# Kernel optimization log

Measured on AMD Instinct MI355X. Metric: run time of the kernel, lower is better.

Reference implementation:

```python
import jax, jax.numpy as jnp
import numpy as np

WIN = (9, 9)
EPS = float(np.power(np.e, -15))  # e^-15 threshold from original code


def _box_sum(x, win):
    kernel = jnp.ones((1, 1, win[0], win[1]), dtype=x.dtype)
    p = win[0] // 2
    return jax.lax.conv_general_dilated(
        x, kernel, window_strides=(1, 1), padding=[(p, p), (p, p)],
        dimension_numbers=("NCHW", "OIHW", "NCHW"))


def setup_inputs() -> dict:
    key = jax.random.key(0)
    k1, k2 = jax.random.split(key)
    B, C, H, W = 32, 1, 512, 512
    I = jax.random.normal(k1, (B, C, H, W), dtype=jnp.float32)
    J = jax.random.normal(k2, (B, C, H, W), dtype=jnp.float32)
    return {"I": I, "J": J}


def reference(I, J):
    win = WIN
    win_size = win[0] * win[1]
    I_sum = _box_sum(I, win)
    J_sum = _box_sum(J, win)
    I2_sum = _box_sum(I * I, win)
    J2_sum = _box_sum(J * J, win)
    IJ_sum = _box_sum(I * J, win)

    u_I = I_sum / win_size
    u_J = J_sum / win_size
    cross = IJ_sum - u_J * I_sum - u_I * J_sum + u_I * u_J * win_size
    I_var = I2_sum - 2 * u_I * I_sum + u_I * u_I * win_size
    J_var = J2_sum - 2 * u_J * J_sum + u_J * u_J * win_size

    non_zero = I_var * J_var > EPS
    cross = jnp.where(non_zero, cross, 1.0)
    I_var = jnp.where(non_zero, I_var, 1.0)
    J_var = jnp.where(non_zero, J_var, 1.0)

    cc = cross * cross / (I_var * J_var + EPS)
    return -1.0 * jnp.mean(cc, axis=(1, 2, 3)) + 1.0
```

## Files before the change

### kernel.cpp

```cpp
#include <hip/hip_runtime.h>


#define IMG_H 512
#define IMG_W 512
#define NBATCH 32
#define RPW 16
#define STRIPS_PER_IMG (IMG_H / RPW)
#define RING 10

typedef __attribute__((address_space(3))) void       lds_t;
typedef __attribute__((address_space(1))) const void glob_t;

__global__ __launch_bounds__(64, 1) void lcc_main(const float* __restrict__ I,
                                                  const float* __restrict__ J,
                                                  float* __restrict__ out) {
    __shared__ __align__(16) float ring[RING][1024];

    const int lane  = threadIdx.x;
    const int strip = blockIdx.x;
    const int b  = strip >> 5;
    const int y0 = (strip & 31) * RPW;
    const int x0 = lane * 8;

    const float* __restrict__ Ib = I + (size_t)b * IMG_H * IMG_W;
    const float* __restrict__ Jb = J + (size_t)b * IMG_H * IMG_W;

    auto issue_row = [&](int y) {
        int slot = (y - y0 + 4) % RING;
        const float* gI = Ib + y * IMG_W;
        const float* gJ = Jb + y * IMG_W;
        float* lI = &ring[slot][0];
        float* lJ = &ring[slot][512];
        __builtin_amdgcn_global_load_lds((glob_t*)(gI +       lane * 4), (lds_t*)lI,         16, 0, 0);
        __builtin_amdgcn_global_load_lds((glob_t*)(gI + 256 + lane * 4), (lds_t*)(lI + 256), 16, 0, 0);
        __builtin_amdgcn_global_load_lds((glob_t*)(gJ +       lane * 4), (lds_t*)lJ,         16, 0, 0);
        __builtin_amdgcn_global_load_lds((glob_t*)(gJ + 256 + lane * 4), (lds_t*)(lJ + 256), 16, 0, 0);
    };

    float sI[8]  = {0.f,0.f,0.f,0.f,0.f,0.f,0.f,0.f};
    float sJ[8]  = {0.f,0.f,0.f,0.f,0.f,0.f,0.f,0.f};
    float sII[8] = {0.f,0.f,0.f,0.f,0.f,0.f,0.f,0.f};
    float sJJ[8] = {0.f,0.f,0.f,0.f,0.f,0.f,0.f,0.f};
    float sIJ[8] = {0.f,0.f,0.f,0.f,0.f,0.f,0.f,0.f};

    auto add_ld = [&](int y) {
        int slot = (y - y0 + 4) % RING;
        const float4* pI = reinterpret_cast<const float4*>(&ring[slot][x0]);
        const float4* pJ = reinterpret_cast<const float4*>(&ring[slot][512 + x0]);
        float4 i0 = pI[0], i1 = pI[1], j0 = pJ[0], j1 = pJ[1];
        float iv[8] = {i0.x,i0.y,i0.z,i0.w,i1.x,i1.y,i1.z,i1.w};
        float jv[8] = {j0.x,j0.y,j0.z,j0.w,j1.x,j1.y,j1.z,j1.w};
        #pragma unroll
        for (int c = 0; c < 8; ++c) {
            sI[c]  += iv[c];
            sJ[c]  += jv[c];
            sII[c]  = fmaf(iv[c], iv[c], sII[c]);
            sJJ[c]  = fmaf(jv[c], jv[c], sJJ[c]);
            sIJ[c]  = fmaf(iv[c], jv[c], sIJ[c]);
        }
    };
    auto sub_ld = [&](int y) {
        int slot = (y - y0 + 4) % RING;
        const float4* pI = reinterpret_cast<const float4*>(&ring[slot][x0]);
        const float4* pJ = reinterpret_cast<const float4*>(&ring[slot][512 + x0]);
        float4 i0 = pI[0], i1 = pI[1], j0 = pJ[0], j1 = pJ[1];
        float iv[8] = {i0.x,i0.y,i0.z,i0.w,i1.x,i1.y,i1.z,i1.w};
        float jv[8] = {j0.x,j0.y,j0.z,j0.w,j1.x,j1.y,j1.z,j1.w};
        #pragma unroll
        for (int c = 0; c < 8; ++c) {
            sI[c]  -= iv[c];
            sJ[c]  -= jv[c];
            sII[c]  = fmaf(-iv[c], iv[c], sII[c]);
            sJJ[c]  = fmaf(-jv[c], jv[c], sJJ[c]);
            sIJ[c]  = fmaf(-iv[c], jv[c], sIJ[c]);
        }
    };

    auto hsum = [&](const float (&s)[8], float (&h)[8]) {
        float w[16];
        #pragma unroll
        for (int c = 0; c < 8; ++c) w[4+c] = s[c];
        #pragma unroll
        for (int c = 0; c < 4; ++c) {
            float a = __shfl_up(s[4+c], 1);
            w[c] = lane ? a : 0.f;
            a = __shfl_down(s[c], 1);
            w[12+c] = (lane < 63) ? a : 0.f;
        }
        float acc = 0.f;
        #pragma unroll
        for (int i = 0; i < 9; ++i) acc += w[i];
        h[0] = acc;
        #pragma unroll
        for (int k = 1; k < 8; ++k) { acc += w[k+8] - w[k-1]; h[k] = acc; }
    };

    const int wy_lo = (y0 - 4 < 0) ? 0 : y0 - 4;
    const int wy_hi = y0 + 4;
    #pragma unroll 1
    for (int y = wy_lo; y <= wy_hi; ++y) issue_row(y);
    __builtin_amdgcn_s_waitcnt(0x3F70);
    #pragma unroll 1
    for (int y = wy_lo; y <= wy_hi; ++y) add_ld(y);

    const float inv81 = 1.0f / 81.0f;
    const float EPSV  = 3.0590232050182579e-07f;
    float local = 0.0f;

    #pragma unroll 1
    for (int r = 0; r < RPW; ++r) {
        const int t = y0 + r;

        const bool pf = (r + 1 < RPW) && (t + 5 < IMG_H);
        if (pf) {
            __builtin_amdgcn_s_waitcnt(0xC07F);
            issue_row(t + 5);
        }

        float hI[8], hJ[8], hII[8], hJJ[8], hIJ[8];
        hsum(sI,  hI);
        hsum(sJ,  hJ);
        hsum(sII, hII);
        hsum(sJJ, hJJ);
        hsum(sIJ, hIJ);

        #pragma unroll
        for (int k = 0; k < 8; ++k) {
            float cross = fmaf(hI[k] * hJ[k], -inv81, hIJ[k]);
            float Iv    = fmaf(hI[k] * hI[k], -inv81, hII[k]);
            float Jv    = fmaf(hJ[k] * hJ[k], -inv81, hJJ[k]);
            float p  = Iv * Jv;
            bool  nz = p > EPSV;
            float c2 = nz ? cross : 1.0f;
            float p2 = nz ? p : 1.0f;
            local += (c2 * c2) * __builtin_amdgcn_rcpf(p2 + EPSV);
        }

        if (r + 1 < RPW) {
            if (pf) __builtin_amdgcn_s_waitcnt(0x3F70);
            if (t + 5 < IMG_H) add_ld(t + 5);
            if (t - 4 >= 0)    sub_ld(t - 4);
        }
    }

    #pragma unroll
    for (int off = 32; off > 0; off >>= 1) local += __shfl_down(local, off);
    if (lane == 0)
        atomicAdd(out + b, fmaf(local, -1.0f / (float)(IMG_H * IMG_W),
                                1.0f / (float)STRIPS_PER_IMG));
}

extern "C" void kernel_launch(void* const* d_in, const int* in_sizes, int n_in,
                              void* d_out, int out_size, void* d_ws, size_t ws_size,
                              hipStream_t stream) {
    const float* I = (const float*)d_in[0];
    const float* J = (const float*)d_in[1];
    float* out = (float*)d_out;

    const int total_strips = NBATCH * STRIPS_PER_IMG;
    lcc_main<<<total_strips, 64, 0, stream>>>(I, J, out);
}
```

Measured before the change: 108.0 us.

## Split each strip across two waves with LDS halo columns and barriers

Each block now runs 128 threads. Each of the two waves handles 256 columns at 4 columns per lane instead of one wave handling 512 columns at 8 per lane. The lane at each half's boundary keeps extra running sums for the 4 halo columns read from the shared LDS ring. Only wave 0 issues the global-to-LDS row loads, and __syncthreads replaces the per-wave waitcnt so wave 1 sees the data. The goal is more waves per CU and half the per-wave arithmetic and register use, at the cost of two block barriers per row and some divergent edge-lane work.

```diff
diff --git a/kernel.cpp b/kernel.cpp
--- a/kernel.cpp
+++ b/kernel.cpp
@@ -11,16 +11,21 @@
 typedef __attribute__((address_space(3))) void       lds_t;
 typedef __attribute__((address_space(1))) const void glob_t;
 
-__global__ __launch_bounds__(64, 1) void lcc_main(const float* __restrict__ I,
-                                                  const float* __restrict__ J,
-                                                  float* __restrict__ out) {
+__global__ __launch_bounds__(128, 2) void lcc_main(const float* __restrict__ I,
+                                                   const float* __restrict__ J,
+                                                   float* __restrict__ out) {
     __shared__ __align__(16) float ring[RING][1024];
 
-    const int lane  = threadIdx.x;
+    const int tid   = threadIdx.x;
+    const int lane  = tid & 63;
+    const int wid   = tid >> 6;
     const int strip = blockIdx.x;
     const int b  = strip >> 5;
     const int y0 = (strip & 31) * RPW;
-    const int x0 = lane * 8;
+    const int cb = (wid << 8) + lane * 4;
+    const bool w0 = (wid == 0);
+    const int elane = w0 ? 63 : 0;
+    const int ecol  = w0 ? 256 : 252;
 
     const float* __restrict__ Ib = I + (size_t)b * IMG_H * IMG_W;
     const float* __restrict__ Jb = J + (size_t)b * IMG_H * IMG_W;
@@ -37,69 +42,97 @@
         __builtin_amdgcn_global_load_lds((glob_t*)(gJ + 256 + lane * 4), (lds_t*)(lJ + 256), 16, 0, 0);
     };
 
-    float sI[8]  = {0.f,0.f,0.f,0.f,0.f,0.f,0.f,0.f};
-    float sJ[8]  = {0.f,0.f,0.f,0.f,0.f,0.f,0.f,0.f};
-    float sII[8] = {0.f,0.f,0.f,0.f,0.f,0.f,0.f,0.f};
-    float sJJ[8] = {0.f,0.f,0.f,0.f,0.f,0.f,0.f,0.f};
-    float sIJ[8] = {0.f,0.f,0.f,0.f,0.f,0.f,0.f,0.f};
+    float sI[4]={0,0,0,0}, sJ[4]={0,0,0,0}, sII[4]={0,0,0,0},
+          sJJ[4]={0,0,0,0}, sIJ[4]={0,0,0,0};
+    float eI[4]={0,0,0,0}, eJ[4]={0,0,0,0}, eII[4]={0,0,0,0},
+          eJJ[4]={0,0,0,0}, eIJ[4]={0,0,0,0};
 
     auto add_ld = [&](int y) {
         int slot = (y - y0 + 4) % RING;
-        const float4* pI = reinterpret_cast<const float4*>(&ring[slot][x0]);
-        const float4* pJ = reinterpret_cast<const float4*>(&ring[slot][512 + x0]);
-        float4 i0 = pI[0], i1 = pI[1], j0 = pJ[0], j1 = pJ[1];
-        float iv[8] = {i0.x,i0.y,i0.z,i0.w,i1.x,i1.y,i1.z,i1.w};
-        float jv[8] = {j0.x,j0.y,j0.z,j0.w,j1.x,j1.y,j1.z,j1.w};
+        float4 i0 = *reinterpret_cast<const float4*>(&ring[slot][cb]);
+        float4 j0 = *reinterpret_cast<const float4*>(&ring[slot][512 + cb]);
+        float iv[4] = {i0.x,i0.y,i0.z,i0.w};
+        float jv[4] = {j0.x,j0.y,j0.z,j0.w};
         #pragma unroll
-        for (int c = 0; c < 8; ++c) {
+        for (int c = 0; c < 4; ++c) {
             sI[c]  += iv[c];
             sJ[c]  += jv[c];
             sII[c]  = fmaf(iv[c], iv[c], sII[c]);
             sJJ[c]  = fmaf(jv[c], jv[c], sJJ[c]);
             sIJ[c]  = fmaf(iv[c], jv[c], sIJ[c]);
         }
+        if (lane == elane) {
+            float4 hi = *reinterpret_cast<const float4*>(&ring[slot][ecol]);
+            float4 hj = *reinterpret_cast<const float4*>(&ring[slot][512 + ecol]);
+            float xi[4] = {hi.x,hi.y,hi.z,hi.w};
+            float xj[4] = {hj.x,hj.y,hj.z,hj.w};
+            #pragma unroll
+            for (int c = 0; c < 4; ++c) {
+                eI[c]  += xi[c];
+                eJ[c]  += xj[c];
+                eII[c]  = fmaf(xi[c], xi[c], eII[c]);
+                eJJ[c]  = fmaf(xj[c], xj[c], eJJ[c]);
+                eIJ[c]  = fmaf(xi[c], xj[c], eIJ[c]);
+            }
+        }
     };
     auto sub_ld = [&](int y) {
         int slot = (y - y0 + 4) % RING;
-        const float4* pI = reinterpret_cast<const float4*>(&ring[slot][x0]);
-        const float4* pJ = reinterpret_cast<const float4*>(&ring[slot][512 + x0]);
-        float4 i0 = pI[0], i1 = pI[1], j0 = pJ[0], j1 = pJ[1];
-        float iv[8] = {i0.x,i0.y,i0.z,i0.w,i1.x,i1.y,i1.z,i1.w};
-        float jv[8] = {j0.x,j0.y,j0.z,j0.w,j1.x,j1.y,j1.z,j1.w};
+        float4 i0 = *reinterpret_cast<const float4*>(&ring[slot][cb]);
+        float4 j0 = *reinterpret_cast<const float4*>(&ring[slot][512 + cb]);
+        float iv[4] = {i0.x,i0.y,i0.z,i0.w};
+        float jv[4] = {j0.x,j0.y,j0.z,j0.w};
         #pragma unroll
-        for (int c = 0; c < 8; ++c) {
+        for (int c = 0; c < 4; ++c) {
             sI[c]  -= iv[c];
             sJ[c]  -= jv[c];
             sII[c]  = fmaf(-iv[c], iv[c], sII[c]);
             sJJ[c]  = fmaf(-jv[c], jv[c], sJJ[c]);
             sIJ[c]  = fmaf(-iv[c], jv[c], sIJ[c]);
         }
+        if (lane == elane) {
+            float4 hi = *reinterpret_cast<const float4*>(&ring[slot][ecol]);
+            float4 hj = *reinterpret_cast<const float4*>(&ring[slot][512 + ecol]);
+            float xi[4] = {hi.x,hi.y,hi.z,hi.w};
+            float xj[4] = {hj.x,hj.y,hj.z,hj.w};
+            #pragma unroll
+            for (int c = 0; c < 4; ++c) {
+                eI[c]  -= xi[c];
+                eJ[c]  -= xj[c];
+                eII[c]  = fmaf(-xi[c], xi[c], eII[c]);
+                eJJ[c]  = fmaf(-xj[c], xj[c], eJJ[c]);
+                eIJ[c]  = fmaf(-xi[c], xj[c], eIJ[c]);
+            }
+        }
     };
 
-    auto hsum = [&](const float (&s)[8], float (&h)[8]) {
-        float w[16];
-        #pragma unroll
-        for (int c = 0; c < 8; ++c) w[4+c] = s[c];
+    auto hsum = [&](const float (&s)[4], const float (&e)[4], float (&h)[4]) {
+        float w[12];
+        w[4]=s[0]; w[5]=s[1]; w[6]=s[2]; w[7]=s[3];
         #pragma unroll
         for (int c = 0; c < 4; ++c) {
-            float a = __shfl_up(s[4+c], 1);
-            w[c] = lane ? a : 0.f;
-            a = __shfl_down(s[c], 1);
-            w[12+c] = (lane < 63) ? a : 0.f;
+            float u = __shfl_up(s[c], 1);
+            float d = __shfl_down(s[c], 1);
+            w[c]   = w0 ? (lane ? u : 0.f)
+                        : (lane ? u : e[c]);
+            w[8+c] = w0 ? ((lane < 63) ? d : e[c])
+                        : ((lane < 63) ? d : 0.f);
         }
         float acc = 0.f;
         #pragma unroll
         for (int i = 0; i < 9; ++i) acc += w[i];
         h[0] = acc;
         #pragma unroll
-        for (int k = 1; k < 8; ++k) { acc += w[k+8] - w[k-1]; h[k] = acc; }
+        for (int k = 1; k < 4; ++k) { acc += w[k+8] - w[k-1]; h[k] = acc; }
     };
 
     const int wy_lo = (y0 - 4 < 0) ? 0 : y0 - 4;
     const int wy_hi = y0 + 4;
-    #pragma unroll 1
-    for (int y = wy_lo; y <= wy_hi; ++y) issue_row(y);
-    __builtin_amdgcn_s_waitcnt(0x3F70);
+    if (w0) {
+        #pragma unroll 1
+        for (int y = wy_lo; y <= wy_hi; ++y) issue_row(y);
+    }
+    __syncthreads();
     #pragma unroll 1
     for (int y = wy_lo; y <= wy_hi; ++y) add_ld(y);
 
@@ -110,22 +143,22 @@
     #pragma unroll 1
     for (int r = 0; r < RPW; ++r) {
         const int t = y0 + r;
+        const bool pf = (r + 1 < RPW) && (t + 5 < IMG_H);
 
-        const bool pf = (r + 1 < RPW) && (t + 5 < IMG_H);
-        if (pf) {
+        if (pf && w0) {
             __builtin_amdgcn_s_waitcnt(0xC07F);
             issue_row(t + 5);
         }
 
-        float hI[8], hJ[8], hII[8], hJJ[8], hIJ[8];
-        hsum(sI,  hI);
-        hsum(sJ,  hJ);
-        hsum(sII, hII);
-        hsum(sJJ, hJJ);
-        hsum(sIJ, hIJ);
+        float hI[4], hJ[4], hII[4], hJJ[4], hIJ[4];
+        hsum(sI,  eI,  hI);
+        hsum(sJ,  eJ,  hJ);
+        hsum(sII, eII, hII);
+        hsum(sJJ, eJJ, hJJ);
+        hsum(sIJ, eIJ, hIJ);
 
         #pragma unroll
-        for (int k = 0; k < 8; ++k) {
+        for (int k = 0; k < 4; ++k) {
             float cross = fmaf(hI[k] * hJ[k], -inv81, hIJ[k]);
             float Iv    = fmaf(hI[k] * hI[k], -inv81, hII[k]);
             float Jv    = fmaf(hJ[k] * hJ[k], -inv81, hJJ[k]);
@@ -137,9 +170,12 @@
         }
 
         if (r + 1 < RPW) {
-            if (pf) __builtin_amdgcn_s_waitcnt(0x3F70);
-            if (t + 5 < IMG_H) add_ld(t + 5);
-            if (t - 4 >= 0)    sub_ld(t - 4);
+            if (t + 5 < IMG_H) {
+                __syncthreads();
+                add_ld(t + 5);
+            }
+            if (t - 4 >= 0) sub_ld(t - 4);
+            __syncthreads();
         }
     }
 
@@ -147,7 +183,7 @@
     for (int off = 32; off > 0; off >>= 1) local += __shfl_down(local, off);
     if (lane == 0)
         atomicAdd(out + b, fmaf(local, -1.0f / (float)(IMG_H * IMG_W),
-                                1.0f / (float)STRIPS_PER_IMG));
+                                1.0f / (float)(STRIPS_PER_IMG * 2)));
 }
 
 extern "C" void kernel_launch(void* const* d_in, const int* in_sizes, int n_in,
@@ -158,5 +194,5 @@
     float* out = (float*)d_out;
 
     const int total_strips = NBATCH * STRIPS_PER_IMG;
-    lcc_main<<<total_strips, 64, 0, stream>>>(I, J, out);
+    lcc_main<<<total_strips, 128, 0, stream>>>(I, J, out);
 }
```

Result: slower. 124.2 us (+15.0%).
